# Kernel tuning notes

Hardware: AMD Instinct MI355X
Metric: run time of the kernel (lower is better)

The kernel has to match this reference:

```python
import jax, jax.numpy as jnp
import numpy as np
from jax import lax

EPS = 1e-5


def _poly_ste(x):
    # polynomial STE: forward sign(x), backward piecewise-polynomial surrogate
    s = jnp.sign(x)
    out1 = jnp.where(x < -1.0, -1.0, x * x + 2.0 * x)
    out2 = jnp.where(x < 0.0, out1, -x * x + 2.0 * x)
    out3 = jnp.where(x < 1.0, out2, 1.0)
    return lax.stop_gradient(s - out3) + out3


def _binary_conv(x, w, stride):
    # per-filter scale (detached) * sign(w), STE through clipped weights
    scale = lax.stop_gradient(jnp.mean(jnp.abs(w), axis=(1, 2, 3), keepdims=True))
    wc = jnp.clip(w, -1.0, 1.0)
    bw = lax.stop_gradient(scale * jnp.sign(w) - wc) + wc
    return lax.conv_general_dilated(
        x, bw, window_strides=(stride, stride), padding=[(1, 1), (1, 1)],
        dimension_numbers=('NCHW', 'OIHW', 'NCHW'))


def _bn_train(x, gamma, beta):
    mu = jnp.mean(x, axis=(0, 2, 3), keepdims=True)
    var = jnp.var(x, axis=(0, 2, 3), keepdims=True)  # biased, as torch BN normalization
    return gamma.reshape(1, -1, 1, 1) * (x - mu) * lax.rsqrt(var + EPS) + beta.reshape(1, -1, 1, 1)


def _prelu(x, a):
    a = a.reshape(1, -1, 1, 1)
    return jnp.where(x >= 0, x, a * x)


def setup_inputs() -> dict:
    key = jax.random.key(0)
    ks = jax.random.split(key, 16)
    N, C, H, W = 64, 256, 28, 28
    P = 256  # planes
    d = {}
    d['x'] = jax.random.normal(ks[0], (N, C, H, W), jnp.float32)
    # LearnableBias params (init zeros in torch; small random to exercise math)
    d['b10'] = jax.random.normal(ks[1], (1, C, 1, 1), jnp.float32) * 0.01
    d['w1'] = jax.random.uniform(ks[2], (P, C, 3, 3), jnp.float32) * 0.001
    d['gamma1'] = 1.0 + 0.1 * jax.random.normal(ks[3], (P,), jnp.float32)
    d['beta1'] = 0.1 * jax.random.normal(ks[4], (P,), jnp.float32)
    d['b11'] = jax.random.normal(ks[5], (1, P, 1, 1), jnp.float32) * 0.01
    d['a1'] = 0.25 + 0.01 * jax.random.normal(ks[6], (P,), jnp.float32)
    d['b12'] = jax.random.normal(ks[7], (1, P, 1, 1), jnp.float32) * 0.01
    d['b20'] = jax.random.normal(ks[8], (1, P, 1, 1), jnp.float32) * 0.01
    d['w2'] = jax.random.uniform(ks[9], (P, P, 3, 3), jnp.float32) * 0.001
    d['gamma2'] = 1.0 + 0.1 * jax.random.normal(ks[10], (P,), jnp.float32)
    d['beta2'] = 0.1 * jax.random.normal(ks[11], (P,), jnp.float32)
    d['b21'] = jax.random.normal(ks[12], (1, P, 1, 1), jnp.float32) * 0.01
    d['a2'] = 0.25 + 0.01 * jax.random.normal(ks[13], (P,), jnp.float32)
    d['b22'] = jax.random.normal(ks[14], (1, P, 1, 1), jnp.float32) * 0.01
    return d


def reference(x, b10, w1, gamma1, beta1, b11, a1, b12,
              b20, w2, gamma2, beta2, b21, a2, b22):
    stride = 1
    residual = x
    h = x + b10
    h = _poly_ste(h)
    h = _binary_conv(h, w1, stride)
    h = _bn_train(h, gamma1, beta1)
    h = h + residual
    h = h + b11
    h = _prelu(h, a1)
    h = h + b12
    y = h + b20
    y = _poly_ste(y)
    y = _binary_conv(y, w2, stride)
    y = _bn_train(y, gamma2, beta2)
    y = y + h
    y = y + b21
    y = _prelu(y, a2)
    y = y + b22
    return y
```

## Files before the change

### kernel.cpp

```cpp
#include <hip/hip_runtime.h>

using i32x4 = __attribute__((ext_vector_type(4))) int;

#define OFF_SCALES 0u
#define OFF_AB     4096u
#define OFF_WPK1   14336u
#define OFF_WPK2   604160u
#define OFF_SPAD   1193984u
#define OFF_COUT   15939584u

__device__ __forceinline__ char sgn8(float v) {
  return v > 0.f ? (char)1 : (v < 0.f ? (char)-1 : (char)0);
}

__global__ __launch_bounds__(256) void k_wprep2(const float* __restrict__ w,
                                                char* __restrict__ wp,
                                                float* __restrict__ sc) {
  int o = blockIdx.x, c = threadIdx.x;
  const float* wr = w + ((size_t)o * 256 + c) * 9;
  int base = ((c >> 6) * 16384) + ((o >> 4) * 1024) +
             (((o & 15) + (((c >> 4) & 3) << 4)) << 4) + (c & 15);
  float s = 0.f;
#pragma unroll
  for (int khw = 0; khw < 9; ++khw) {
    float v = wr[khw];
    s += fabsf(v);
    wp[khw * 65536 + base] = sgn8(v);
  }
  for (int m = 1; m < 64; m <<= 1) s += __shfl_xor(s, m);
  __shared__ float red[4];
  if ((c & 63) == 0) red[c >> 6] = s;
  __syncthreads();
  if (c == 0) sc[o] = (red[0] + red[1] + red[2] + red[3]) * (1.f / 2304.f);
}

__global__ __launch_bounds__(512) void k_e0(const float* __restrict__ x,
                                            const float* __restrict__ b10,
                                            char* __restrict__ sp) {
  __shared__ char lds[112 * 260];
  int img = blockIdx.x / 7, y4 = blockIdx.x % 7;
  int y0 = y4 * 4;
  int t = threadIdx.x;
  int r = t & 31;
  int cb = t >> 5;
  if (r < 28) {
    int p0 = r * 4;
    for (int ci = 0; ci < 16; ++ci) {
      int c = ci * 16 + cb;
      float vb = b10[c];
      size_t off = ((size_t)(img * 256 + c) * 28 + y0) * 28 + p0;
      float4 xv = *reinterpret_cast<const float4*>(x + off);
      char* lp = &lds[p0 * 260 + c];
      lp[0]   = sgn8(xv.x + vb);
      lp[260] = sgn8(xv.y + vb);
      lp[520] = sgn8(xv.z + vb);
      lp[780] = sgn8(xv.w + vb);
    }
  }
  __syncthreads();
#pragma unroll
  for (int row = 0; row < 4; ++row) {
    size_t bse = (((size_t)img * 30 + (y0 + row + 1)) * 30 + 1) * 256;
    int* spi = (int*)(sp + bse);
    for (int q = t; q < 1792; q += 512) {
      int xo = q >> 6, c4 = (q & 63) << 2;
      spi[q] = *(const int*)&lds[(row * 28 + xo) * 260 + c4];
    }
  }
  {
    int row = t >> 7, rem = t & 127;
    int col = (rem & 1) * 29, c4w = rem >> 1;
    ((int*)&sp[(((size_t)img * 30 + (y0 + row + 1)) * 30 + col) * 256])[c4w] = 0;
  }
  if (y4 == 0)
    for (int q = t; q < 1920; q += 512)
      ((int*)&sp[(size_t)img * 230400])[q] = 0;
  if (y4 == 6)
    for (int q = t; q < 1920; q += 512)
      ((int*)&sp[(size_t)img * 230400 + 29 * 7680])[q] = 0;
}

__global__ __launch_bounds__(512, 4) void k_conv(const char* __restrict__ S,
                                                 const char* __restrict__ Wp,
                                                 short* __restrict__ C) {
  __shared__ char lds[46080];
  int bid = blockIdx.x;
  int img = bid / 7;
  int yt  = bid % 7;
  int tid = threadIdx.x;
  int wave = tid >> 6, lane = tid & 63;
  int l15 = lane & 15, lg = lane >> 4;
  int y0 = yt * 4;

  const char* sb = S + (size_t)img * 230400 + (size_t)y0 * 7680;
  for (int q = tid; q < 2880; q += 512) {
    int tp = q >> 4;
    int g  = q & 15;
    int k  = (tp - 2 * (tp / 30)) & 15;
    int4 v = *reinterpret_cast<const int4*>(sb + tp * 256 + g * 16);
    *reinterpret_cast<int4*>(&lds[tp * 256 + ((g ^ k) << 4)]) = v;
  }
  __syncthreads();

  int pixtp[7];
#pragma unroll
  for (int j = 0; j < 7; ++j) {
    int p = j * 16 + l15;
    pixtp[j] = (p / 28) * 30 + (p % 28);
  }
  i32x4 acc[2][7] = {};

#pragma unroll 1
  for (int kh = 0; kh < 3; ++kh) {
#pragma unroll
    for (int kw = 0; kw < 3; ++kw) {
      int khw = kh * 3 + kw;
      int shift = kh * 30 + kw;
      int kk = (l15 + 12 * kh + kw) & 15;
      const char* ab = Wp + (size_t)khw * 65536 + (size_t)wave * 2048 + lane * 16;
#pragma unroll
      for (int cc = 0; cc < 4; ++cc) {
        i32x4 afr[2];
        afr[0] = *reinterpret_cast<const i32x4*>(ab + cc * 16384);
        afr[1] = *reinterpret_cast<const i32x4*>(ab + cc * 16384 + 1024);
        int gr = (lg + 4 * cc) ^ kk;
        i32x4 bfr[7];
#pragma unroll
        for (int j = 0; j < 7; ++j) {
          int tp = pixtp[j] + shift;
          bfr[j] = *reinterpret_cast<const i32x4*>(&lds[tp * 256 + (gr << 4)]);
        }
#pragma unroll
        for (int mi = 0; mi < 2; ++mi)
#pragma unroll
          for (int j = 0; j < 7; ++j)
            acc[mi][j] = __builtin_amdgcn_mfma_i32_16x16x64_i8(afr[mi], bfr[j], acc[mi][j], 0, 0, 0);
      }
    }
  }

  short* cb = C + (size_t)img * 200704;
#pragma unroll
  for (int mi = 0; mi < 2; ++mi) {
#pragma unroll
    for (int r = 0; r < 4; ++r) {
      int o = wave * 32 + mi * 16 + lg * 4 + r;
#pragma unroll
      for (int j = 0; j < 7; ++j) {
        int p = j * 16 + l15;
        cb[(size_t)o * 784 + (y0 + p / 28) * 28 + (p % 28)] = (short)acc[mi][j][r];
      }
    }
  }
}

__global__ __launch_bounds__(256) void k_stats(const short* __restrict__ C,
                                               const float* __restrict__ scale,
                                               const float* __restrict__ gamma,
                                               const float* __restrict__ beta,
                                               float* __restrict__ AB) {
  int o = blockIdx.x, t = threadIdx.x;
  int s1 = 0;
  long long s2 = 0;
  for (int q = t; q < 64 * 98; q += 256) {
    int img = q / 98, r = q - img * 98;
    int4 v = *reinterpret_cast<const int4*>(C + (size_t)img * 200704 + o * 784 + r * 8);
    short vs[8];
    *reinterpret_cast<int4*>(vs) = v;
#pragma unroll
    for (int e = 0; e < 8; ++e) {
      int xv = vs[e];
      s1 += xv;
      s2 += (long long)xv * xv;
    }
  }
  for (int m = 1; m < 64; m <<= 1) {
    s1 += __shfl_xor(s1, m);
    s2 += __shfl_xor(s2, m);
  }
  __shared__ int rs1[4];
  __shared__ long long rs2[4];
  if ((t & 63) == 0) { rs1[t >> 6] = s1; rs2[t >> 6] = s2; }
  __syncthreads();
  if (t == 0) {
    long long S1 = (long long)rs1[0] + rs1[1] + rs1[2] + rs1[3];
    long long S2 = rs2[0] + rs2[1] + rs2[2] + rs2[3];
    double n  = 50176.0;
    double sc = (double)scale[o];
    double mI = (double)S1 / n;
    double vI = (double)S2 / n - mI * mI;
    double mu  = sc * mI;
    double var = sc * sc * vI;
    double rr = 1.0 / sqrt(var + 1e-5);
    double g = (double)gamma[o];
    AB[o]       = (float)(g * sc * rr);
    AB[256 + o] = (float)((double)beta[o] - g * rr * mu);
  }
}

__global__ __launch_bounds__(512) void k_e1(const short* __restrict__ c1,
                                            const float* __restrict__ x,
                                            const float* __restrict__ AB,
                                            const float* __restrict__ b11,
                                            const float* __restrict__ a1,
                                            const float* __restrict__ b12,
                                            const float* __restrict__ b20,
                                            float* __restrict__ ho,
                                            char* __restrict__ sp) {
  __shared__ char lds[112 * 260];
  int img = blockIdx.x / 7, y4 = blockIdx.x % 7;
  int y0 = y4 * 4;
  int t = threadIdx.x;
  int r = t & 31;
  int cb = t >> 5;
  if (r < 28) {
    int p0 = r * 4;
    for (int ci = 0; ci < 16; ++ci) {
      int c = ci * 16 + cb;
      float A = AB[c], B = AB[256 + c];
      float v11 = b11[c], va = a1[c], v12 = b12[c], v20 = b20[c];
      size_t off = ((size_t)(img * 256 + c) * 28 + y0) * 28 + p0;
      float4 xv = *reinterpret_cast<const float4*>(x + off);
      short4 cv = *reinterpret_cast<const short4*>(c1 + off);
      float h0 = A * (float)cv.x + B + xv.x + v11; h0 = h0 >= 0.f ? h0 : va * h0; h0 += v12;
      float h1 = A * (float)cv.y + B + xv.y + v11; h1 = h1 >= 0.f ? h1 : va * h1; h1 += v12;
      float h2 = A * (float)cv.z + B + xv.z + v11; h2 = h2 >= 0.f ? h2 : va * h2; h2 += v12;
      float h3 = A * (float)cv.w + B + xv.w + v11; h3 = h3 >= 0.f ? h3 : va * h3; h3 += v12;
      float4 hv; hv.x = h0; hv.y = h1; hv.z = h2; hv.w = h3;
      *reinterpret_cast<float4*>(ho + off) = hv;
      char* lp = &lds[p0 * 260 + c];
      lp[0]   = sgn8(h0 + v20);
      lp[260] = sgn8(h1 + v20);
      lp[520] = sgn8(h2 + v20);
      lp[780] = sgn8(h3 + v20);
    }
  }
  __syncthreads();
#pragma unroll
  for (int row = 0; row < 4; ++row) {
    size_t bse = (((size_t)img * 30 + (y0 + row + 1)) * 30 + 1) * 256;
    int* spi = (int*)(sp + bse);
    for (int q = t; q < 1792; q += 512) {
      int xo = q >> 6, c4 = (q & 63) << 2;
      spi[q] = *(const int*)&lds[(row * 28 + xo) * 260 + c4];
    }
  }
}

__global__ __launch_bounds__(256) void k_e2(const short* __restrict__ c2,
                                            const float* __restrict__ AB2,
                                            const float* __restrict__ b21,
                                            const float* __restrict__ a2,
                                            const float* __restrict__ b22,
                                            float* __restrict__ io) {
  int v = blockIdx.x * 256 + threadIdx.x;
  int c = ((v * 4) / 784) & 255;
  float A = AB2[c], B = AB2[256 + c];
  float p21 = b21[c], aa = a2[c], p22 = b22[c];
  short4 I = reinterpret_cast<const short4*>(c2)[v];
  float4 h = reinterpret_cast<const float4*>(io)[v];
  float4 r;
  float t0 = A * (float)I.x + B + h.x + p21; t0 = t0 >= 0.f ? t0 : aa * t0; r.x = t0 + p22;
  float t1 = A * (float)I.y + B + h.y + p21; t1 = t1 >= 0.f ? t1 : aa * t1; r.y = t1 + p22;
  float t2 = A * (float)I.z + B + h.z + p21; t2 = t2 >= 0.f ? t2 : aa * t2; r.z = t2 + p22;
  float t3 = A * (float)I.w + B + h.w + p21; t3 = t3 >= 0.f ? t3 : aa * t3; r.w = t3 + p22;
  reinterpret_cast<float4*>(io)[v] = r;
}

extern "C" void kernel_launch(void* const* d_in, const int* in_sizes, int n_in,
                              void* d_out, int out_size, void* d_ws, size_t ws_size,
                              hipStream_t stream) {
  const float* x      = (const float*)d_in[0];
  const float* b10    = (const float*)d_in[1];
  const float* w1     = (const float*)d_in[2];
  const float* gamma1 = (const float*)d_in[3];
  const float* beta1  = (const float*)d_in[4];
  const float* b11    = (const float*)d_in[5];
  const float* a1     = (const float*)d_in[6];
  const float* b12    = (const float*)d_in[7];
  const float* b20    = (const float*)d_in[8];
  const float* w2     = (const float*)d_in[9];
  const float* gamma2 = (const float*)d_in[10];
  const float* beta2  = (const float*)d_in[11];
  const float* b21    = (const float*)d_in[12];
  const float* a2     = (const float*)d_in[13];
  const float* b22    = (const float*)d_in[14];
  float* out = (float*)d_out;

  char* ws = (char*)d_ws;
  float* scales = (float*)(ws + OFF_SCALES);
  float* AB     = (float*)(ws + OFF_AB);
  char*  wpk1   = ws + OFF_WPK1;
  char*  wpk2   = ws + OFF_WPK2;
  char*  spad   = ws + OFF_SPAD;
  short* cout   = (short*)(ws + OFF_COUT);

  k_wprep2<<<256, 256, 0, stream>>>(w1, wpk1, scales);
  k_wprep2<<<256, 256, 0, stream>>>(w2, wpk2, scales + 256);

  k_e0<<<448, 512, 0, stream>>>(x, b10, spad);
  k_conv<<<448, 512, 0, stream>>>(spad, wpk1, cout);
  k_stats<<<256, 256, 0, stream>>>(cout, scales, gamma1, beta1, AB);
  k_e1<<<448, 512, 0, stream>>>(cout, x, AB, b11, a1, b12, b20, out, spad);
  k_conv<<<448, 512, 0, stream>>>(spad, wpk2, cout);
  k_stats<<<256, 256, 0, stream>>>(cout, scales + 256, gamma2, beta2, AB + 512);
  k_e2<<<12544, 256, 0, stream>>>(cout, AB + 512, b21, a2, b22, out);
}
```

Before: 151.7 us.

## Fuse BN statistics partial sums into conv epilogue and merge weight prep launches

The conv kernel now computes per-channel partial sums and sums of squares in its epilogue, reducing across the 16-lane groups with shuffles and writing one partial per (channel, block) to a new workspace buffer. The stats kernel then only reduces 448 partials per channel instead of rereading the whole int16 conv output, which removes two full passes over that tensor. The two weight-prep launches are also merged into a single 512-block launch. The cost is extra shuffle work and register pressure in the conv epilogue, and the per-thread sum of squares is now held in 32-bit int.

```diff
diff --git a/kernel.cpp b/kernel.cpp
--- a/kernel.cpp
+++ b/kernel.cpp
@@ -4,19 +4,25 @@
 
 #define OFF_SCALES 0u
 #define OFF_AB     4096u
-#define OFF_WPK1   14336u
-#define OFF_WPK2   604160u
-#define OFF_SPAD   1193984u
-#define OFF_COUT   15939584u
+#define OFF_PBUF   8192u
+#define OFF_WPK1   925696u
+#define OFF_WPK2   1515520u
+#define OFF_SPAD   2105344u
+#define OFF_COUT   16850944u
 
 __device__ __forceinline__ char sgn8(float v) {
   return v > 0.f ? (char)1 : (v < 0.f ? (char)-1 : (char)0);
 }
 
-__global__ __launch_bounds__(256) void k_wprep2(const float* __restrict__ w,
-                                                char* __restrict__ wp,
+__global__ __launch_bounds__(256) void k_wprep2(const float* __restrict__ w1,
+                                                const float* __restrict__ w2,
+                                                char* __restrict__ wp1,
+                                                char* __restrict__ wp2,
                                                 float* __restrict__ sc) {
-  int o = blockIdx.x, c = threadIdx.x;
+  int bid = blockIdx.x;
+  int o = bid & 255, c = threadIdx.x;
+  const float* w = (bid < 256) ? w1 : w2;
+  char* wp = (bid < 256) ? wp1 : wp2;
   const float* wr = w + ((size_t)o * 256 + c) * 9;
   int base = ((c >> 6) * 16384) + ((o >> 4) * 1024) +
              (((o & 15) + (((c >> 4) & 3) << 4)) << 4) + (c & 15);
@@ -31,7 +37,7 @@
   __shared__ float red[4];
   if ((c & 63) == 0) red[c >> 6] = s;
   __syncthreads();
-  if (c == 0) sc[o] = (red[0] + red[1] + red[2] + red[3]) * (1.f / 2304.f);
+  if (c == 0) sc[bid] = (red[0] + red[1] + red[2] + red[3]) * (1.f / 2304.f);
 }
 
 __global__ __launch_bounds__(512) void k_e0(const float* __restrict__ x,
@@ -82,7 +88,8 @@
 
 __global__ __launch_bounds__(512, 4) void k_conv(const char* __restrict__ S,
                                                  const char* __restrict__ Wp,
-                                                 short* __restrict__ C) {
+                                                 short* __restrict__ C,
+                                                 int* __restrict__ P) {
   __shared__ char lds[46080];
   int bid = blockIdx.x;
   int img = bid / 7;
@@ -145,45 +152,48 @@
 #pragma unroll
     for (int r = 0; r < 4; ++r) {
       int o = wave * 32 + mi * 16 + lg * 4 + r;
+      int s1 = 0, s2 = 0;
 #pragma unroll
       for (int j = 0; j < 7; ++j) {
+        int iv = acc[mi][j][r];
         int p = j * 16 + l15;
-        cb[(size_t)o * 784 + (y0 + p / 28) * 28 + (p % 28)] = (short)acc[mi][j][r];
+        cb[(size_t)o * 784 + (y0 + p / 28) * 28 + (p % 28)] = (short)iv;
+        s1 += iv;
+        s2 += iv * iv;
       }
-    }
-  }
-}
-
-__global__ __launch_bounds__(256) void k_stats(const short* __restrict__ C,
-                                               const float* __restrict__ scale,
-                                               const float* __restrict__ gamma,
-                                               const float* __restrict__ beta,
-                                               float* __restrict__ AB) {
+#pragma unroll
+      for (int m = 1; m < 16; m <<= 1) {
+        s1 += __shfl_xor(s1, m);
+        s2 += __shfl_xor(s2, m);
+      }
+      if (l15 == 0) {
+        P[o * 448 + bid] = s1;
+        P[114688 + o * 448 + bid] = s2;
+      }
+    }
+  }
+}
+
+__global__ __launch_bounds__(256) void k_stats2(const int* __restrict__ P,
+                                                const float* __restrict__ scale,
+                                                const float* __restrict__ gamma,
+                                                const float* __restrict__ beta,
+                                                float* __restrict__ AB) {
   int o = blockIdx.x, t = threadIdx.x;
-  int s1 = 0;
-  long long s2 = 0;
-  for (int q = t; q < 64 * 98; q += 256) {
-    int img = q / 98, r = q - img * 98;
-    int4 v = *reinterpret_cast<const int4*>(C + (size_t)img * 200704 + o * 784 + r * 8);
-    short vs[8];
-    *reinterpret_cast<int4*>(vs) = v;
-#pragma unroll
-    for (int e = 0; e < 8; ++e) {
-      int xv = vs[e];
-      s1 += xv;
-      s2 += (long long)xv * xv;
-    }
+  long long s1 = 0, s2 = 0;
+  for (int q = t; q < 448; q += 256) {
+    s1 += P[o * 448 + q];
+    s2 += P[114688 + o * 448 + q];
   }
   for (int m = 1; m < 64; m <<= 1) {
     s1 += __shfl_xor(s1, m);
     s2 += __shfl_xor(s2, m);
   }
-  __shared__ int rs1[4];
-  __shared__ long long rs2[4];
+  __shared__ long long rs1[4], rs2[4];
   if ((t & 63) == 0) { rs1[t >> 6] = s1; rs2[t >> 6] = s2; }
   __syncthreads();
   if (t == 0) {
-    long long S1 = (long long)rs1[0] + rs1[1] + rs1[2] + rs1[3];
+    long long S1 = rs1[0] + rs1[1] + rs1[2] + rs1[3];
     long long S2 = rs2[0] + rs2[1] + rs2[2] + rs2[3];
     double n  = 50176.0;
     double sc = (double)scale[o];
@@ -290,19 +300,19 @@
   char* ws = (char*)d_ws;
   float* scales = (float*)(ws + OFF_SCALES);
   float* AB     = (float*)(ws + OFF_AB);
+  int*   pbuf   = (int*)(ws + OFF_PBUF);
   char*  wpk1   = ws + OFF_WPK1;
   char*  wpk2   = ws + OFF_WPK2;
   char*  spad   = ws + OFF_SPAD;
   short* cout   = (short*)(ws + OFF_COUT);
 
-  k_wprep2<<<256, 256, 0, stream>>>(w1, wpk1, scales);
-  k_wprep2<<<256, 256, 0, stream>>>(w2, wpk2, scales + 256);
+  k_wprep2<<<512, 256, 0, stream>>>(w1, w2, wpk1, wpk2, scales);
 
   k_e0<<<448, 512, 0, stream>>>(x, b10, spad);
-  k_conv<<<448, 512, 0, stream>>>(spad, wpk1, cout);
-  k_stats<<<256, 256, 0, stream>>>(cout, scales, gamma1, beta1, AB);
+  k_conv<<<448, 512, 0, stream>>>(spad, wpk1, cout, pbuf);
+  k_stats2<<<256, 256, 0, stream>>>(pbuf, scales, gamma1, beta1, AB);
   k_e1<<<448, 512, 0, stream>>>(cout, x, AB, b11, a1, b12, b20, out, spad);
-  k_conv<<<448, 512, 0, stream>>>(spad, wpk2, cout);
-  k_stats<<<256, 256, 0, stream>>>(cout, scales + 256, gamma2, beta2, AB + 512);
+  k_conv<<<448, 512, 0, stream>>>(spad, wpk2, cout, pbuf);
+  k_stats2<<<256, 256, 0, stream>>>(pbuf, scales + 256, gamma2, beta2, AB + 512);
   k_e2<<<12544, 256, 0, stream>>>(cout, AB + 512, b21, a2, b22, out);
 }
```

After: 132.6 us, median of 2. 12.6% less time.
